# Optimization experiments

Measured on AMD Instinct MI355X. Metric: run time of the kernel, lower is better.

## Reference

```python
import jax, jax.numpy as jnp
import numpy as np

D_MODEL = 1024
NUM_HEADS = 16
HEAD_DIM = D_MODEL // NUM_HEADS


def setup_inputs() -> dict:
    key = jax.random.key(0)
    ks = jax.random.split(key, 9)
    s = 1.0 / np.sqrt(D_MODEL)
    inp = {"x": jax.random.normal(ks[0], (2, 2048, D_MODEL), dtype=jnp.float32)}
    for i, name in enumerate(["q", "k", "v", "o"]):
        inp[f"W_{name}"] = jax.random.uniform(ks[1 + i], (D_MODEL, D_MODEL), dtype=jnp.float32, minval=-s, maxval=s)
        inp[f"b_{name}"] = jax.random.uniform(ks[5 + i], (D_MODEL,), dtype=jnp.float32, minval=-s, maxval=s)
    return inp


def reference(x, W_q, b_q, W_k, b_k, W_v, b_v, W_o, b_o):
    B, S, _ = x.shape
    def split_heads(t):  # [B,S,D] -> [B,H,S,Dh]
        return t.reshape(B, S, NUM_HEADS, HEAD_DIM).transpose(0, 2, 1, 3)
    q = split_heads(x @ W_q.T + b_q)
    k = split_heads(x @ W_k.T + b_k)
    v = split_heads(x @ W_v.T + b_v)
    scale = 1.0 / np.sqrt(HEAD_DIM).astype(np.float32)
    scores = jnp.einsum('bhqd,bhkd->bhqk', q, k) * scale  # [B,H,S,S]
    attn = jax.nn.softmax(scores, axis=-1)
    out = jnp.einsum('bhqk,bhkd->bhqd', attn, v)  # [B,H,S,Dh]
    out = out.transpose(0, 2, 1, 3).reshape(B, S, D_MODEL)
    return out @ W_o.T + b_o
```

## Files before the change

kernel.cpp:

```cpp
#include <hip/hip_runtime.h>
#include <hip/hip_bf16.h>

typedef __attribute__((ext_vector_type(8))) short short8;
typedef __attribute__((ext_vector_type(4))) float f32x4;
typedef __attribute__((ext_vector_type(16))) float f32x16;
typedef unsigned short ushort_t;
typedef unsigned int uint_t;

#define LOG2E 1.4426950408889634f

#if __has_builtin(__builtin_amdgcn_exp2f)
#define EXP2(x) __builtin_amdgcn_exp2f(x)
#else
#define EXP2(x) exp2f(x)
#endif

__device__ __forceinline__ ushort_t f2bf(float f) {
    union { float f; unsigned int i; } x; x.f = f;
    unsigned int r = x.i + 0x7FFF + ((x.i >> 16) & 1);
    return (ushort_t)(r >> 16);
}
__device__ __forceinline__ float bf2f(ushort_t u) {
    union { unsigned int i; float f; } x; x.i = ((unsigned int)u) << 16; return x.f;
}
__device__ __forceinline__ uint_t cvtpk(float lo, float hi) {
    uint_t r;
    asm("v_cvt_pk_bf16_f32 %0, %1, %2" : "=v"(r) : "v"(lo), "v"(hi));
    return r;
}

__device__ __forceinline__ void gll16(const void* g, void* l) {
    __builtin_amdgcn_global_load_lds((const __attribute__((address_space(1))) unsigned int*)g,
                                     (__attribute__((address_space(3))) unsigned int*)l,
                                     16, 0, 0);
}

__device__ __forceinline__ int xcd_lin() {
    int gx = gridDim.x;
    int n  = gx * gridDim.y;
    int lin = blockIdx.y * gx + blockIdx.x;
    int cpx = n >> 3;
    return (lin & 7) * cpx + (lin >> 3);
}

__global__ __launch_bounds__(256) void convert_kernel(
    const float* __restrict__ x,
    const float* __restrict__ Wq, const float* __restrict__ Wk,
    const float* __restrict__ Wv, const float* __restrict__ Wo,
    const float* __restrict__ bq, const float* __restrict__ bk, const float* __restrict__ bv,
    ushort_t* __restrict__ xb, ushort_t* __restrict__ wqkv,
    ushort_t* __restrict__ wob, float* __restrict__ bqkv)
{
    int idx = blockIdx.x * 256 + threadIdx.x;
    const float* src; ushort_t* dst; int off;
    if (idx < 1048576) { src = x; dst = xb; off = idx * 4; }
    else if (idx < 1835008) {
        int e = (idx - 1048576) * 4;
        int wi = e >> 20; off = e & 1048575;
        src = (wi == 0) ? Wq : ((wi == 1) ? Wk : Wv);
        dst = wqkv + ((size_t)wi << 20);
    } else { off = (idx - 1835008) * 4; src = Wo; dst = wob; }
    float4 v = *reinterpret_cast<const float4*>(src + off);
    ushort_t o0 = f2bf(v.x), o1 = f2bf(v.y), o2 = f2bf(v.z), o3 = f2bf(v.w);
    ushort_t* d = dst + off;
    d[0] = o0; d[1] = o1; d[2] = o2; d[3] = o3;
    if (idx < 768) {
        int wi = idx >> 8; int o4 = (idx & 255) * 4;
        const float* bsrc = (wi == 0) ? bq : ((wi == 1) ? bk : bv);
        *reinterpret_cast<float4*>(bqkv + wi * 1024 + o4) =
            *reinterpret_cast<const float4*>(bsrc + o4);
    }
}

template<int WRITE_BF16, int BN>
__global__ __launch_bounds__(256) void gemm_nt(
    const ushort_t* __restrict__ A, const ushort_t* __restrict__ Bm,
    const float* __restrict__ bias, void* __restrict__ Cout,
    int M, int N, int K)
{
    constexpr int NT = BN / 32;
    __shared__ ushort_t As[2][128 * 32];
    __shared__ ushort_t Bs[2][BN * 32];

    const int tid  = threadIdx.x;
    const int lane = tid & 63;
    const int wv   = tid >> 6;

    const int sw = xcd_lin();
    const int bx = sw % gridDim.x;
    const int by = sw / gridDim.x;
    const int m0 = by * 128;
    const int n0 = bx * BN;

    const int wr   = wv >> 1, wc = wv & 1;
    const int g    = lane >> 4, c = lane & 15;

    f32x4 acc[4][NT] = {};

    const int srow = lane >> 2;
    const int scol = (lane & 3) * 8;
    const ushort_t* Ag = A  + (size_t)(m0 + wv * 32 + srow) * K + scol;
    const ushort_t* Bg = Bm + (size_t)(n0 + (BN == 128 ? wv * 32 : wv * 16) + srow) * K + scol;

    auto STAGE = [&](int b, int k0) {
        gll16(Ag + k0,          &As[b][(wv * 32) * 32]);
        gll16(Ag + 16 * K + k0, &As[b][(wv * 32 + 16) * 32]);
        if (BN == 128) {
            gll16(Bg + k0,          &Bs[b][(wv * 32) * 32]);
            gll16(Bg + 16 * K + k0, &Bs[b][(wv * 32 + 16) * 32]);
        } else {
            gll16(Bg + k0,          &Bs[b][(wv * 16) * 32]);
        }
    };

    STAGE(0, 0);
    __syncthreads();
    int cur = 0;
    for (int k0 = 0; k0 < K; k0 += 32) {
        if (k0 + 32 < K) STAGE(cur ^ 1, k0 + 32);

        short8 af[4], bf[NT];
        #pragma unroll
        for (int i = 0; i < 4; i++)
            af[i] = *reinterpret_cast<const short8*>(&As[cur][(wr * 64 + i * 16 + c) * 32 + g * 8]);
        #pragma unroll
        for (int j = 0; j < NT; j++)
            bf[j] = *reinterpret_cast<const short8*>(&Bs[cur][(wc * (BN / 2) + j * 16 + c) * 32 + g * 8]);
        #pragma unroll
        for (int i = 0; i < 4; i++)
            #pragma unroll
            for (int j = 0; j < NT; j++)
                acc[i][j] = __builtin_amdgcn_mfma_f32_16x16x32_bf16(af[i], bf[j], acc[i][j], 0, 0, 0);

        __syncthreads();
        cur ^= 1;
    }

    #pragma unroll
    for (int i = 0; i < 4; i++) {
        int row = m0 + wr * 64 + i * 16 + 4 * g;
        #pragma unroll
        for (int j = 0; j < NT; j++) {
            int col = n0 + wc * (BN / 2) + j * 16 + c;
            float bv_ = bias[col];
            #pragma unroll
            for (int r = 0; r < 4; r++) {
                float v = acc[i][j][r] + bv_;
                if (WRITE_BF16)
                    ((ushort_t*)Cout)[(size_t)(row + r) * N + col] = f2bf(v);
                else
                    ((float*)Cout)[(size_t)(row + r) * N + col] = v;
            }
        }
    }
}

__global__ __launch_bounds__(256) void vtrans_kernel(
    const ushort_t* __restrict__ qkv, ushort_t* __restrict__ Vt)
{
    __shared__ ushort_t T[256 * 64];
    const int tid = threadIdx.x;
    const int st0 = blockIdx.x * 256;
    const int bh  = blockIdx.y;
    const int b = bh >> 4, h = bh & 15;
    const ushort_t* vg = qkv + (size_t)b * 2048 * 3072 + 2048 + h * 64;

    #pragma unroll
    for (int p = 0; p < 8; p++) {
        int tok = p * 32 + (tid >> 3);
        int ch  = (tid & 7) ^ (tok & 7);
        short8 v = *reinterpret_cast<const short8*>(
            vg + (size_t)(st0 + tok) * 3072 + (tid & 7) * 8);
        *reinterpret_cast<short8*>(&T[tok * 64 + ch * 8]) = v;
    }
    __syncthreads();
    const int d = tid >> 2;
    ushort_t* og = Vt + ((size_t)bh * 64 + d) * 2048 + st0;
    #pragma unroll
    for (int it = 0; it < 8; it++) {
        int sc_ = (tid & 3) + 4 * it;
        short8 v;
        #pragma unroll
        for (int e = 0; e < 8; e++) {
            int s = sc_ * 8 + e;
            v[e] = (short)T[s * 64 + (((d >> 3) ^ (s & 7)) * 8) + (d & 7)];
        }
        *reinterpret_cast<short8*>(og + sc_ * 8) = v;
    }
}

__global__ __launch_bounds__(256) void attn_kernel(
    const ushort_t* __restrict__ qkv, const ushort_t* __restrict__ Vt,
    ushort_t* __restrict__ out)
{
    __shared__ ushort_t smem[32768];

    const int tid  = threadIdx.x;
    const int lane = tid & 63;
    const int wv   = tid >> 6;
    const int sw   = xcd_lin();
    const int qt   = sw & 15;
    const int bh   = sw >> 4;
    const int b = bh >> 4, h = bh & 15;
    const int c  = lane & 31;
    const int hh = lane >> 5;

    const int q0 = qt * 128 + wv * 32;
    const size_t tokbase = (size_t)b * 2048;

    short8 qf[4];
    {
        const ushort_t* qg = qkv + (tokbase + q0 + c) * 3072 + h * 64 + hh * 8;
        #pragma unroll
        for (int s = 0; s < 4; s++) {
            short8 v = *reinterpret_cast<const short8*>(qg + s * 16);
            short8 o;
            #pragma unroll
            for (int e = 0; e < 8; e++)
                o[e] = (short)f2bf(bf2f((ushort_t)v[e]) * (0.125f * LOG2E));
            qf[s] = o;
        }
    }

    const int l8  = lane & 7;
    const int l3  = lane >> 3;
    const int ldr = lane >> 4;
    const int l16h = (lane >> 3) & 1;
    const ushort_t* kg0 = qkv + (tokbase + wv * 32 + l3) * 3072 + 1024 + h * 64 + (l8 ^ l3) * 8;
    const ushort_t* vgA = Vt + ((size_t)bh * 64 + wv * 16 + ldr) * 2048 + (l16h * 8 + (l8 ^ ldr)) * 8;
    const ushort_t* vgB = Vt + ((size_t)bh * 64 + wv * 16 + ldr) * 2048 + (l16h * 8 + (l8 ^ (ldr ^ 4))) * 8;

    f32x16 oacc[2] = {};
    f32x16 sc[4];
    float l0 = 0.f, l1 = 0.f, l2 = 0.f, l3s = 0.f;

    auto STAGE = [&](int bb, int kt) {
        char* Kd = (char*)smem + bb * 32768 + wv * 4096;
        char* Vd = (char*)smem + bb * 32768 + 16384 + wv * 4096;
        const ushort_t* ks = kg0 + (size_t)(kt * 128) * 3072;
        gll16(ks,                         Kd);
        gll16(ks + (size_t)8  * 3072,     Kd + 1024);
        gll16(ks + (size_t)16 * 3072,     Kd + 2048);
        gll16(ks + (size_t)24 * 3072,     Kd + 3072);
        const ushort_t* vs0 = vgA + kt * 128;
        const ushort_t* vs1 = vgB + kt * 128;
        gll16(vs0,             Vd);
        gll16(vs1 + 4 * 2048,  Vd + 1024);
        gll16(vs0 + 8 * 2048,  Vd + 2048);
        gll16(vs1 + 12 * 2048, Vd + 3072);
    };

    STAGE(0, 0);
    __syncthreads();
    int cur = 0;

    for (int it = 0; it < 16; it++) {
        if (it + 1 < 16) STAGE(cur ^ 1, it + 1);

        const char* KlB = (const char*)smem + cur * 32768;
        const char* VlB = KlB + 16384;

        sc[0] = f32x16{}; sc[1] = f32x16{}; sc[2] = f32x16{}; sc[3] = f32x16{};
        __builtin_amdgcn_s_setprio(1);
        #pragma unroll
        for (int st = 0; st < 4; st++) {
            int chB = (((2 * st + hh) ^ (c & 7)) << 4);
            short8 ak0 = *reinterpret_cast<const short8*>(KlB + (c     ) * 128 + chB);
            short8 ak1 = *reinterpret_cast<const short8*>(KlB + (32 + c) * 128 + chB);
            short8 ak2 = *reinterpret_cast<const short8*>(KlB + (64 + c) * 128 + chB);
            short8 ak3 = *reinterpret_cast<const short8*>(KlB + (96 + c) * 128 + chB);
            sc[0] = __builtin_amdgcn_mfma_f32_32x32x16_bf16(ak0, qf[st], sc[0], 0, 0, 0);
            sc[1] = __builtin_amdgcn_mfma_f32_32x32x16_bf16(ak1, qf[st], sc[1], 0, 0, 0);
            sc[2] = __builtin_amdgcn_mfma_f32_32x32x16_bf16(ak2, qf[st], sc[2], 0, 0, 0);
            sc[3] = __builtin_amdgcn_mfma_f32_32x32x16_bf16(ak3, qf[st], sc[3], 0, 0, 0);
        }
        __builtin_amdgcn_s_setprio(0);

        #pragma unroll
        for (int t = 0; t < 4; t++) {
            #pragma unroll
            for (int r = 0; r < 16; r += 4) {
                sc[t][r]   = EXP2(sc[t][r]);   l0  += sc[t][r];
                sc[t][r+1] = EXP2(sc[t][r+1]); l1  += sc[t][r+1];
                sc[t][r+2] = EXP2(sc[t][r+2]); l2  += sc[t][r+2];
                sc[t][r+3] = EXP2(sc[t][r+3]); l3s += sc[t][r+3];
            }
        }

        __builtin_amdgcn_s_setprio(1);
        #pragma unroll
        for (int s = 0; s < 8; s++) {
            const int t0 = s >> 1;
            const int rb = (s & 1) * 8;
            uint_t A0 = cvtpk(sc[t0][rb + 0], sc[t0][rb + 1]);
            uint_t B0 = cvtpk(sc[t0][rb + 2], sc[t0][rb + 3]);
            uint_t A1 = cvtpk(sc[t0][rb + 4], sc[t0][rb + 5]);
            uint_t B1 = cvtpk(sc[t0][rb + 6], sc[t0][rb + 7]);
            uint_t sendA = hh ? A0 : A1;
            uint_t sendB = hh ? B0 : B1;
            uint_t recvA = (uint_t)__shfl_xor((int)sendA, 32);
            uint_t recvB = (uint_t)__shfl_xor((int)sendB, 32);
            uint_t d0 = hh ? recvA : A0;
            uint_t d1 = hh ? recvB : B0;
            uint_t d2 = hh ? A1 : recvA;
            uint_t d3 = hh ? B1 : recvB;
            union { uint_t u[4]; short8 s8; } pu;
            pu.u[0] = d0; pu.u[1] = d1; pu.u[2] = d2; pu.u[3] = d3;

            const int chB = (s >> 2) * 128 + (((2 * (s & 3) + hh) ^ (c & 7)) << 4);
            short8 av0 = *reinterpret_cast<const short8*>(VlB + (c     ) * 256 + chB);
            short8 av1 = *reinterpret_cast<const short8*>(VlB + (32 + c) * 256 + chB);
            oacc[0] = __builtin_amdgcn_mfma_f32_32x32x16_bf16(av0, pu.s8, oacc[0], 0, 0, 0);
            oacc[1] = __builtin_amdgcn_mfma_f32_32x32x16_bf16(av1, pu.s8, oacc[1], 0, 0, 0);
        }
        __builtin_amdgcn_s_setprio(0);

        __syncthreads();
        cur ^= 1;
    }

    float l_own = (l0 + l1) + (l2 + l3s);
    float l_tot = l_own + __shfl_xor(l_own, 32);
    float invl = 1.0f / l_tot;

    ushort_t* Olw = smem + wv * 32 * 72;
    #pragma unroll
    for (int td = 0; td < 2; td++)
        #pragma unroll
        for (int rr = 0; rr < 4; rr++)
            #pragma unroll
            for (int j2 = 0; j2 < 2; j2++) {
                int r = 4 * rr + 2 * j2;
                float v0 = (td == 0) ? oacc[0][r] : oacc[1][r];
                float v1 = (td == 0) ? oacc[0][r + 1] : oacc[1][r + 1];
                uint_t wd = cvtpk(v0 * invl, v1 * invl);
                int dcol = 32 * td + 4 * hh + 8 * rr + 2 * j2;
                *reinterpret_cast<uint_t*>(&Olw[c * 72 + dcol]) = wd;
            }
    __syncthreads();
    {
        int row = lane >> 1;
        int e0  = (lane & 1) * 32;
        const ushort_t* Olr = smem + wv * 32 * 72;
        ushort_t* og = out + (tokbase + q0 + row) * 1024 + h * 64 + e0;
        #pragma unroll
        for (int k2 = 0; k2 < 4; k2++) {
            short8 v;
            #pragma unroll
            for (int e = 0; e < 8; e++) v[e] = (short)Olr[row * 72 + e0 + k2 * 8 + e];
            *reinterpret_cast<short8*>(og + k2 * 8) = v;
        }
    }
}

extern "C" void kernel_launch(void* const* d_in, const int* in_sizes, int n_in,
                              void* d_out, int out_size, void* d_ws, size_t ws_size,
                              hipStream_t stream) {
    const float* x  = (const float*)d_in[0];
    const float* Wq = (const float*)d_in[1];
    const float* bq = (const float*)d_in[2];
    const float* Wk = (const float*)d_in[3];
    const float* bk = (const float*)d_in[4];
    const float* Wv = (const float*)d_in[5];
    const float* bv = (const float*)d_in[6];
    const float* Wo = (const float*)d_in[7];
    const float* bo = (const float*)d_in[8];

    uintptr_t w = (uintptr_t)d_ws;
    ushort_t* xb    = (ushort_t*)w;  w += 8388608;
    ushort_t* wqkv  = (ushort_t*)w;  w += 6291456;
    ushort_t* wob   = (ushort_t*)w;  w += 2097152;
    float*    bqkv  = (float*)w;     w += 12288;
    ushort_t* qkv   = (ushort_t*)w;  w += 25165824;
    ushort_t* attno = (ushort_t*)w;  w += 8388608;
    ushort_t* Vt    = xb;

    convert_kernel<<<8192, 256, 0, stream>>>(x, Wq, Wk, Wv, Wo, bq, bk, bv,
                                             xb, wqkv, wob, bqkv);
    gemm_nt<1, 128><<<dim3(24, 32), 256, 0, stream>>>(xb, wqkv, bqkv, qkv, 4096, 3072, 1024);
    vtrans_kernel<<<dim3(8, 32), 256, 0, stream>>>(qkv, Vt);
    attn_kernel<<<dim3(16, 32), 256, 0, stream>>>(qkv, Vt, attno);
    gemm_nt<0, 64><<<dim3(16, 32), 256, 0, stream>>>(attno, wob, bo, (void*)d_out, 4096, 1024, 1024);
}
```

Before: 120.4 us.

## Use partial vmcnt waits for double buffering and interleave QK/exp/PV per tile

In both the GEMM and attention loops, the blanket __syncthreads after each prefetch becomes explicit s_waitcnt vmcnt(N) plus a raw s_barrier. Each iteration now waits only for the current buffer's global-to-LDS loads while the next buffer's loads stay in flight. The attention inner loop is also restructured to process each 32-key subtile fully (QK MFMA, exp2, PV MFMA) before the next, instead of computing all scores first. This cuts live registers from four score accumulators to one and lets exp work overlap MFMAs. The hand-coded vmcnt counts must match the exact number of issued loads, or a race results.

```diff
diff --git a/kernel.cpp b/kernel.cpp
--- a/kernel.cpp
+++ b/kernel.cpp
@@ -114,10 +114,18 @@
     };
 
     STAGE(0, 0);
-    __syncthreads();
     int cur = 0;
     for (int k0 = 0; k0 < K; k0 += 32) {
-        if (k0 + 32 < K) STAGE(cur ^ 1, k0 + 32);
+        if (k0 + 32 < K) {
+            STAGE(cur ^ 1, k0 + 32);
+            if (BN == 128) asm volatile("s_waitcnt vmcnt(4)" ::: "memory");
+            else           asm volatile("s_waitcnt vmcnt(3)" ::: "memory");
+        } else {
+            asm volatile("s_waitcnt vmcnt(0)" ::: "memory");
+        }
+        __builtin_amdgcn_sched_barrier(0);
+        __builtin_amdgcn_s_barrier();
+        __builtin_amdgcn_sched_barrier(0);
 
         short8 af[4], bf[NT];
         #pragma unroll
@@ -132,7 +140,10 @@
             for (int j = 0; j < NT; j++)
                 acc[i][j] = __builtin_amdgcn_mfma_f32_16x16x32_bf16(af[i], bf[j], acc[i][j], 0, 0, 0);
 
-        __syncthreads();
+        asm volatile("s_waitcnt lgkmcnt(0)" ::: "memory");
+        __builtin_amdgcn_sched_barrier(0);
+        __builtin_amdgcn_s_barrier();
+        __builtin_amdgcn_sched_barrier(0);
         cur ^= 1;
     }
 
@@ -231,7 +242,6 @@
     const ushort_t* vgB = Vt + ((size_t)bh * 64 + wv * 16 + ldr) * 2048 + (l16h * 8 + (l8 ^ (ldr ^ 4))) * 8;
 
     f32x16 oacc[2] = {};
-    f32x16 sc[4];
     float l0 = 0.f, l1 = 0.f, l2 = 0.f, l3s = 0.f;
 
     auto STAGE = [&](int bb, int kt) {
@@ -251,71 +261,71 @@
     };
 
     STAGE(0, 0);
-    __syncthreads();
     int cur = 0;
 
     for (int it = 0; it < 16; it++) {
-        if (it + 1 < 16) STAGE(cur ^ 1, it + 1);
+        if (it + 1 < 16) {
+            STAGE(cur ^ 1, it + 1);
+            asm volatile("s_waitcnt vmcnt(8)" ::: "memory");
+        } else {
+            asm volatile("s_waitcnt vmcnt(0)" ::: "memory");
+        }
+        __builtin_amdgcn_sched_barrier(0);
+        __builtin_amdgcn_s_barrier();
+        __builtin_amdgcn_sched_barrier(0);
 
         const char* KlB = (const char*)smem + cur * 32768;
         const char* VlB = KlB + 16384;
 
-        sc[0] = f32x16{}; sc[1] = f32x16{}; sc[2] = f32x16{}; sc[3] = f32x16{};
         __builtin_amdgcn_s_setprio(1);
         #pragma unroll
-        for (int st = 0; st < 4; st++) {
-            int chB = (((2 * st + hh) ^ (c & 7)) << 4);
-            short8 ak0 = *reinterpret_cast<const short8*>(KlB + (c     ) * 128 + chB);
-            short8 ak1 = *reinterpret_cast<const short8*>(KlB + (32 + c) * 128 + chB);
-            short8 ak2 = *reinterpret_cast<const short8*>(KlB + (64 + c) * 128 + chB);
-            short8 ak3 = *reinterpret_cast<const short8*>(KlB + (96 + c) * 128 + chB);
-            sc[0] = __builtin_amdgcn_mfma_f32_32x32x16_bf16(ak0, qf[st], sc[0], 0, 0, 0);
-            sc[1] = __builtin_amdgcn_mfma_f32_32x32x16_bf16(ak1, qf[st], sc[1], 0, 0, 0);
-            sc[2] = __builtin_amdgcn_mfma_f32_32x32x16_bf16(ak2, qf[st], sc[2], 0, 0, 0);
-            sc[3] = __builtin_amdgcn_mfma_f32_32x32x16_bf16(ak3, qf[st], sc[3], 0, 0, 0);
+        for (int t = 0; t < 4; t++) {
+            f32x16 s = {};
+            #pragma unroll
+            for (int st = 0; st < 4; st++) {
+                const int chB = (((2 * st + hh) ^ (c & 7)) << 4);
+                short8 ak = *reinterpret_cast<const short8*>(KlB + (32 * t + c) * 128 + chB);
+                s = __builtin_amdgcn_mfma_f32_32x32x16_bf16(ak, qf[st], s, 0, 0, 0);
+            }
+            #pragma unroll
+            for (int r = 0; r < 16; r += 4) {
+                s[r]   = EXP2(s[r]);   l0  += s[r];
+                s[r+1] = EXP2(s[r+1]); l1  += s[r+1];
+                s[r+2] = EXP2(s[r+2]); l2  += s[r+2];
+                s[r+3] = EXP2(s[r+3]); l3s += s[r+3];
+            }
+            #pragma unroll
+            for (int half = 0; half < 2; half++) {
+                const int sidx = 2 * t + half;
+                const int rb = half * 8;
+                uint_t A0 = cvtpk(s[rb + 0], s[rb + 1]);
+                uint_t B0 = cvtpk(s[rb + 2], s[rb + 3]);
+                uint_t A1 = cvtpk(s[rb + 4], s[rb + 5]);
+                uint_t B1 = cvtpk(s[rb + 6], s[rb + 7]);
+                uint_t sendA = hh ? A0 : A1;
+                uint_t sendB = hh ? B0 : B1;
+                uint_t recvA = (uint_t)__shfl_xor((int)sendA, 32);
+                uint_t recvB = (uint_t)__shfl_xor((int)sendB, 32);
+                uint_t d0 = hh ? recvA : A0;
+                uint_t d1 = hh ? recvB : B0;
+                uint_t d2 = hh ? A1 : recvA;
+                uint_t d3 = hh ? B1 : recvB;
+                union { uint_t u[4]; short8 s8; } pu;
+                pu.u[0] = d0; pu.u[1] = d1; pu.u[2] = d2; pu.u[3] = d3;
+
+                const int chB = (sidx >> 2) * 128 + (((2 * (sidx & 3) + hh) ^ (c & 7)) << 4);
+                short8 av0 = *reinterpret_cast<const short8*>(VlB + (c     ) * 256 + chB);
+                short8 av1 = *reinterpret_cast<const short8*>(VlB + (32 + c) * 256 + chB);
+                oacc[0] = __builtin_amdgcn_mfma_f32_32x32x16_bf16(av0, pu.s8, oacc[0], 0, 0, 0);
+                oacc[1] = __builtin_amdgcn_mfma_f32_32x32x16_bf16(av1, pu.s8, oacc[1], 0, 0, 0);
+            }
         }
         __builtin_amdgcn_s_setprio(0);
 
-        #pragma unroll
-        for (int t = 0; t < 4; t++) {
-            #pragma unroll
-            for (int r = 0; r < 16; r += 4) {
-                sc[t][r]   = EXP2(sc[t][r]);   l0  += sc[t][r];
-                sc[t][r+1] = EXP2(sc[t][r+1]); l1  += sc[t][r+1];
-                sc[t][r+2] = EXP2(sc[t][r+2]); l2  += sc[t][r+2];
-                sc[t][r+3] = EXP2(sc[t][r+3]); l3s += sc[t][r+3];
-            }
-        }
-
-        __builtin_amdgcn_s_setprio(1);
-        #pragma unroll
-        for (int s = 0; s < 8; s++) {
-            const int t0 = s >> 1;
-            const int rb = (s & 1) * 8;
-            uint_t A0 = cvtpk(sc[t0][rb + 0], sc[t0][rb + 1]);
-            uint_t B0 = cvtpk(sc[t0][rb + 2], sc[t0][rb + 3]);
-            uint_t A1 = cvtpk(sc[t0][rb + 4], sc[t0][rb + 5]);
-            uint_t B1 = cvtpk(sc[t0][rb + 6], sc[t0][rb + 7]);
-            uint_t sendA = hh ? A0 : A1;
-            uint_t sendB = hh ? B0 : B1;
-            uint_t recvA = (uint_t)__shfl_xor((int)sendA, 32);
-            uint_t recvB = (uint_t)__shfl_xor((int)sendB, 32);
-            uint_t d0 = hh ? recvA : A0;
-            uint_t d1 = hh ? recvB : B0;
-            uint_t d2 = hh ? A1 : recvA;
-            uint_t d3 = hh ? B1 : recvB;
-            union { uint_t u[4]; short8 s8; } pu;
-            pu.u[0] = d0; pu.u[1] = d1; pu.u[2] = d2; pu.u[3] = d3;
-
-            const int chB = (s >> 2) * 128 + (((2 * (s & 3) + hh) ^ (c & 7)) << 4);
-            short8 av0 = *reinterpret_cast<const short8*>(VlB + (c     ) * 256 + chB);
-            short8 av1 = *reinterpret_cast<const short8*>(VlB + (32 + c) * 256 + chB);
-            oacc[0] = __builtin_amdgcn_mfma_f32_32x32x16_bf16(av0, pu.s8, oacc[0], 0, 0, 0);
-            oacc[1] = __builtin_amdgcn_mfma_f32_32x32x16_bf16(av1, pu.s8, oacc[1], 0, 0, 0);
-        }
-        __builtin_amdgcn_s_setprio(0);
-
-        __syncthreads();
+        asm volatile("s_waitcnt lgkmcnt(0)" ::: "memory");
+        __builtin_amdgcn_sched_barrier(0);
+        __builtin_amdgcn_s_barrier();
+        __builtin_amdgcn_sched_barrier(0);
         cur ^= 1;
     }
 
```

Measured after the change: 122.5 us. About the same (+1.7%).

## Split attention KV range across two wave groups and tighten GEMM pipeline waits

Applied to the files above, without the earlier changes.

The attention kernel now launches 512 threads per block. Two groups of four waves each process half of the key/value sequence with smaller 64-key tiles, then combine partial output accumulators and row sums through shared memory before normalizing. This raises wave-level parallelism and latency hiding per query tile, at the cost of an extra LDS reduction and register-pressure limits from the launch bounds. The GEMM main loop replaces __syncthreads with explicit vmcnt/lgkmcnt waits and raw barriers, so the prefetch of the next K slice can stay in flight while the current one is consumed.

```diff
diff --git a/kernel.cpp b/kernel.cpp
--- a/kernel.cpp
+++ b/kernel.cpp
@@ -114,10 +114,18 @@
     };
 
     STAGE(0, 0);
-    __syncthreads();
     int cur = 0;
     for (int k0 = 0; k0 < K; k0 += 32) {
-        if (k0 + 32 < K) STAGE(cur ^ 1, k0 + 32);
+        if (k0 + 32 < K) {
+            STAGE(cur ^ 1, k0 + 32);
+            if (BN == 128) asm volatile("s_waitcnt vmcnt(4)" ::: "memory");
+            else           asm volatile("s_waitcnt vmcnt(3)" ::: "memory");
+        } else {
+            asm volatile("s_waitcnt vmcnt(0)" ::: "memory");
+        }
+        __builtin_amdgcn_sched_barrier(0);
+        __builtin_amdgcn_s_barrier();
+        __builtin_amdgcn_sched_barrier(0);
 
         short8 af[4], bf[NT];
         #pragma unroll
@@ -132,7 +140,10 @@
             for (int j = 0; j < NT; j++)
                 acc[i][j] = __builtin_amdgcn_mfma_f32_16x16x32_bf16(af[i], bf[j], acc[i][j], 0, 0, 0);
 
-        __syncthreads();
+        asm volatile("s_waitcnt lgkmcnt(0)" ::: "memory");
+        __builtin_amdgcn_sched_barrier(0);
+        __builtin_amdgcn_s_barrier();
+        __builtin_amdgcn_sched_barrier(0);
         cur ^= 1;
     }
 
@@ -189,7 +200,7 @@
     }
 }
 
-__global__ __launch_bounds__(256) void attn_kernel(
+__global__ __launch_bounds__(512, 4) void attn_kernel(
     const ushort_t* __restrict__ qkv, const ushort_t* __restrict__ Vt,
     ushort_t* __restrict__ out)
 {
@@ -198,6 +209,8 @@
     const int tid  = threadIdx.x;
     const int lane = tid & 63;
     const int wv   = tid >> 6;
+    const int wvi  = wv & 3;
+    const int g2   = wv >> 2;
     const int sw   = xcd_lin();
     const int qt   = sw & 15;
     const int bh   = sw >> 4;
@@ -205,7 +218,7 @@
     const int c  = lane & 31;
     const int hh = lane >> 5;
 
-    const int q0 = qt * 128 + wv * 32;
+    const int q0 = qt * 128 + wvi * 32;
     const size_t tokbase = (size_t)b * 2048;
 
     short8 qf[4];
@@ -222,32 +235,26 @@
         }
     }
 
-    const int l8  = lane & 7;
-    const int l3  = lane >> 3;
-    const int ldr = lane >> 4;
-    const int l16h = (lane >> 3) & 1;
-    const ushort_t* kg0 = qkv + (tokbase + wv * 32 + l3) * 3072 + 1024 + h * 64 + (l8 ^ l3) * 8;
-    const ushort_t* vgA = Vt + ((size_t)bh * 64 + wv * 16 + ldr) * 2048 + (l16h * 8 + (l8 ^ ldr)) * 8;
-    const ushort_t* vgB = Vt + ((size_t)bh * 64 + wv * 16 + ldr) * 2048 + (l16h * 8 + (l8 ^ (ldr ^ 4))) * 8;
+    const int l8 = lane & 7;
+    const int l3 = lane >> 3;
+    const ushort_t* kg0 = qkv + (tokbase + g2 * 1024 + wvi * 16 + l3) * 3072
+                              + 1024 + h * 64 + (l8 ^ l3) * 8;
+    const ushort_t* vg0 = Vt + ((size_t)bh * 64 + wvi * 16 + l3) * 2048
+                             + g2 * 1024 + (l8 ^ l3) * 8;
 
     f32x16 oacc[2] = {};
-    f32x16 sc[4];
+    f32x16 sc[2];
     float l0 = 0.f, l1 = 0.f, l2 = 0.f, l3s = 0.f;
 
     auto STAGE = [&](int bb, int kt) {
-        char* Kd = (char*)smem + bb * 32768 + wv * 4096;
-        char* Vd = (char*)smem + bb * 32768 + 16384 + wv * 4096;
-        const ushort_t* ks = kg0 + (size_t)(kt * 128) * 3072;
-        gll16(ks,                         Kd);
-        gll16(ks + (size_t)8  * 3072,     Kd + 1024);
-        gll16(ks + (size_t)16 * 3072,     Kd + 2048);
-        gll16(ks + (size_t)24 * 3072,     Kd + 3072);
-        const ushort_t* vs0 = vgA + kt * 128;
-        const ushort_t* vs1 = vgB + kt * 128;
-        gll16(vs0,             Vd);
-        gll16(vs1 + 4 * 2048,  Vd + 1024);
-        gll16(vs0 + 8 * 2048,  Vd + 2048);
-        gll16(vs1 + 12 * 2048, Vd + 3072);
+        char* Kd = (char*)smem + g2 * 32768 + bb * 16384 + wvi * 2048;
+        char* Vd = Kd + 8192;
+        const ushort_t* ks = kg0 + (size_t)(kt * 64) * 3072;
+        gll16(ks,                     Kd);
+        gll16(ks + (size_t)8 * 3072,  Kd + 1024);
+        const ushort_t* vs = vg0 + kt * 64;
+        gll16(vs,            Vd);
+        gll16(vs + 8 * 2048, Vd + 1024);
     };
 
     STAGE(0, 0);
@@ -257,27 +264,23 @@
     for (int it = 0; it < 16; it++) {
         if (it + 1 < 16) STAGE(cur ^ 1, it + 1);
 
-        const char* KlB = (const char*)smem + cur * 32768;
-        const char* VlB = KlB + 16384;
-
-        sc[0] = f32x16{}; sc[1] = f32x16{}; sc[2] = f32x16{}; sc[3] = f32x16{};
+        const char* KlB = (const char*)smem + g2 * 32768 + cur * 16384;
+        const char* VlB = KlB + 8192;
+
+        sc[0] = f32x16{}; sc[1] = f32x16{};
         __builtin_amdgcn_s_setprio(1);
         #pragma unroll
         for (int st = 0; st < 4; st++) {
-            int chB = (((2 * st + hh) ^ (c & 7)) << 4);
+            const int chB = (((2 * st + hh) ^ (c & 7)) << 4);
             short8 ak0 = *reinterpret_cast<const short8*>(KlB + (c     ) * 128 + chB);
             short8 ak1 = *reinterpret_cast<const short8*>(KlB + (32 + c) * 128 + chB);
-            short8 ak2 = *reinterpret_cast<const short8*>(KlB + (64 + c) * 128 + chB);
-            short8 ak3 = *reinterpret_cast<const short8*>(KlB + (96 + c) * 128 + chB);
             sc[0] = __builtin_amdgcn_mfma_f32_32x32x16_bf16(ak0, qf[st], sc[0], 0, 0, 0);
             sc[1] = __builtin_amdgcn_mfma_f32_32x32x16_bf16(ak1, qf[st], sc[1], 0, 0, 0);
-            sc[2] = __builtin_amdgcn_mfma_f32_32x32x16_bf16(ak2, qf[st], sc[2], 0, 0, 0);
-            sc[3] = __builtin_amdgcn_mfma_f32_32x32x16_bf16(ak3, qf[st], sc[3], 0, 0, 0);
         }
         __builtin_amdgcn_s_setprio(0);
 
         #pragma unroll
-        for (int t = 0; t < 4; t++) {
+        for (int t = 0; t < 2; t++) {
             #pragma unroll
             for (int r = 0; r < 16; r += 4) {
                 sc[t][r]   = EXP2(sc[t][r]);   l0  += sc[t][r];
@@ -289,7 +292,7 @@
 
         __builtin_amdgcn_s_setprio(1);
         #pragma unroll
-        for (int s = 0; s < 8; s++) {
+        for (int s = 0; s < 4; s++) {
             const int t0 = s >> 1;
             const int rb = (s & 1) * 8;
             uint_t A0 = cvtpk(sc[t0][rb + 0], sc[t0][rb + 1]);
@@ -307,9 +310,9 @@
             union { uint_t u[4]; short8 s8; } pu;
             pu.u[0] = d0; pu.u[1] = d1; pu.u[2] = d2; pu.u[3] = d3;
 
-            const int chB = (s >> 2) * 128 + (((2 * (s & 3) + hh) ^ (c & 7)) << 4);
-            short8 av0 = *reinterpret_cast<const short8*>(VlB + (c     ) * 256 + chB);
-            short8 av1 = *reinterpret_cast<const short8*>(VlB + (32 + c) * 256 + chB);
+            const int chB = (((2 * s + hh) ^ (c & 7)) << 4);
+            short8 av0 = *reinterpret_cast<const short8*>(VlB + (c     ) * 128 + chB);
+            short8 av1 = *reinterpret_cast<const short8*>(VlB + (32 + c) * 128 + chB);
             oacc[0] = __builtin_amdgcn_mfma_f32_32x32x16_bf16(av0, pu.s8, oacc[0], 0, 0, 0);
             oacc[1] = __builtin_amdgcn_mfma_f32_32x32x16_bf16(av1, pu.s8, oacc[1], 0, 0, 0);
         }
@@ -320,34 +323,43 @@
     }
 
     float l_own = (l0 + l1) + (l2 + l3s);
-    float l_tot = l_own + __shfl_xor(l_own, 32);
-    float invl = 1.0f / l_tot;
-
-    ushort_t* Olw = smem + wv * 32 * 72;
-    #pragma unroll
-    for (int td = 0; td < 2; td++)
-        #pragma unroll
-        for (int rr = 0; rr < 4; rr++)
-            #pragma unroll
-            for (int j2 = 0; j2 < 2; j2++) {
-                int r = 4 * rr + 2 * j2;
-                float v0 = (td == 0) ? oacc[0][r] : oacc[1][r];
-                float v1 = (td == 0) ? oacc[0][r + 1] : oacc[1][r + 1];
-                uint_t wd = cvtpk(v0 * invl, v1 * invl);
-                int dcol = 32 * td + 4 * hh + 8 * rr + 2 * j2;
-                *reinterpret_cast<uint_t*>(&Olw[c * 72 + dcol]) = wd;
-            }
+    float* dump = (float*)smem;
+    const int di = (wvi * 64 + lane) * 34;
+    if (g2) {
+        #pragma unroll
+        for (int r = 0; r < 16; r++) { dump[di + r] = oacc[0][r]; dump[di + 16 + r] = oacc[1][r]; }
+        dump[di + 32] = l_own;
+    }
     __syncthreads();
-    {
+    if (!g2) {
+        #pragma unroll
+        for (int r = 0; r < 16; r++) { oacc[0][r] += dump[di + r]; oacc[1][r] += dump[di + 16 + r]; }
+        l_own += dump[di + 32];
+        float l_tot = l_own + __shfl_xor(l_own, 32);
+        float invl = 1.0f / l_tot;
+
+        ushort_t* Olw = (ushort_t*)((char*)smem + 36864 + wvi * 4608);
+        #pragma unroll
+        for (int td = 0; td < 2; td++)
+            #pragma unroll
+            for (int rr = 0; rr < 4; rr++)
+                #pragma unroll
+                for (int j2 = 0; j2 < 2; j2++) {
+                    int r = 4 * rr + 2 * j2;
+                    float v0 = (td == 0) ? oacc[0][r] : oacc[1][r];
+                    float v1 = (td == 0) ? oacc[0][r + 1] : oacc[1][r + 1];
+                    uint_t wd = cvtpk(v0 * invl, v1 * invl);
+                    int dcol = 32 * td + 4 * hh + 8 * rr + 2 * j2;
+                    *reinterpret_cast<uint_t*>(&Olw[c * 72 + dcol]) = wd;
+                }
         int row = lane >> 1;
         int e0  = (lane & 1) * 32;
-        const ushort_t* Olr = smem + wv * 32 * 72;
         ushort_t* og = out + (tokbase + q0 + row) * 1024 + h * 64 + e0;
         #pragma unroll
         for (int k2 = 0; k2 < 4; k2++) {
             short8 v;
             #pragma unroll
-            for (int e = 0; e < 8; e++) v[e] = (short)Olr[row * 72 + e0 + k2 * 8 + e];
+            for (int e = 0; e < 8; e++) v[e] = (short)Olw[row * 72 + e0 + k2 * 8 + e];
             *reinterpret_cast<short8*>(og + k2 * 8) = v;
         }
     }
@@ -379,6 +391,6 @@
                                              xb, wqkv, wob, bqkv);
     gemm_nt<1, 128><<<dim3(24, 32), 256, 0, stream>>>(xb, wqkv, bqkv, qkv, 4096, 3072, 1024);
     vtrans_kernel<<<dim3(8, 32), 256, 0, stream>>>(qkv, Vt);
-    attn_kernel<<<dim3(16, 32), 256, 0, stream>>>(qkv, Vt, attno);
+    attn_kernel<<<dim3(16, 32), 512, 0, stream>>>(qkv, Vt, attno);
     gemm_nt<0, 64><<<dim3(16, 32), 256, 0, stream>>>(attno, wob, bo, (void*)d_out, 4096, 1024, 1024);
 }
```

Result: faster. 117.2 us (-2.7%).
